# Optimization experiments

Measured on AMD Instinct MI355X. Metric: run time of the kernel, lower is better.

The kernel has to match this reference:

```python
import jax, jax.numpy as jnp
import numpy as np

N_SIN = 3  # fcn_n_sin (static)


def setup_inputs() -> dict:
    key = jax.random.key(0)
    ks = jax.random.split(key, 5)
    B, I, O, H = 256, 128, 128, 32
    F = 1 + 2 * N_SIN
    return {
        "x": jax.random.normal(ks[0], (B, I), dtype=jnp.float32),
        "W1": jax.random.normal(ks[1], (I, O, H, F), dtype=jnp.float32) * 0.3,
        "W2": jax.random.normal(ks[2], (I, O, 1, H), dtype=jnp.float32) * 0.3,
        "B1": jax.random.normal(ks[3], (I, O, H), dtype=jnp.float32) * 0.1,
        "B2": jax.random.normal(ks[4], (I, O, 1), dtype=jnp.float32) * 0.1,
    }


def reference(x, W1, W2, B1, B2):
    # x: [B, I]; per-(i,o) edge MLP on a scalar input, summed over i.
    omega = (2.0 ** jnp.arange(N_SIN)).astype(x.dtype)          # [S]
    ox = x[..., None] * omega                                    # [B, I, S]
    feat = jnp.concatenate([x[..., None], jnp.sin(ox), jnp.cos(ox)], axis=-1)  # [B, I, 1+2S]
    # First linear: per-edge [F -> H]
    h = jnp.einsum('bif,iohf->bioh', feat, W1) + B1              # [B, I, O, H]
    h = jax.nn.silu(h)
    # Second linear: per-edge [H -> 1], then sum over input dims i
    out = jnp.einsum('bioh,ioh->bio', h, W2[:, :, 0, :]) + B2[:, :, 0]  # [B, I, O]
    return out.sum(axis=1)                                       # [B, O]
```

## Files before the change

kernel.cpp:

```cpp
#include <hip/hip_runtime.h>
#include <hip/hip_bf16.h>

#define B_DIM 256
#define I_DIM 128
#define O_DIM 128
#define H_DIM 32
#define F_DIM 7
#define ICHUNK 8
#define NCHUNK (I_DIM / ICHUNK)

typedef __attribute__((ext_vector_type(8))) short short8;
typedef __attribute__((ext_vector_type(4))) float float4v;

__device__ inline short bf16s(float v) {
    union { __hip_bfloat16 h; short s; } u;
    u.h = __float2bfloat16(v);
    return u.s;
}

template <bool USE_WS>
__global__ __launch_bounds__(256, 2)
void fcnkan_mfma(const float* __restrict__ x,
                 const float* __restrict__ W1,
                 const float* __restrict__ W2,
                 const float* __restrict__ B1,
                 const float* __restrict__ B2,
                 float* __restrict__ ws,
                 float* __restrict__ out) {
    __shared__ __align__(16) short feat_s[ICHUNK * B_DIM * 8];
    __shared__ __align__(16) short w1_s[ICHUNK * H_DIM * 8];
    __shared__ float b1_s[ICHUNK * H_DIM];
    __shared__ float w2_s[ICHUNK * H_DIM];

    const int tid  = threadIdx.x;
    const int o    = blockIdx.x;
    const int ic0  = blockIdx.y * ICHUNK;
    const int w    = tid >> 6;
    const int lane = tid & 63;
    const int m    = lane & 15;
    const int q    = lane >> 4;

    const short8 zero8 = {};

    {
        const float4* xp = reinterpret_cast<const float4*>(x + (size_t)tid * I_DIM + ic0);
        float4 x0 = xp[0], x1 = xp[1];
        float xr[8] = {x0.x, x0.y, x0.z, x0.w, x1.x, x1.y, x1.z, x1.w};
        #pragma unroll
        for (int il = 0; il < ICHUNK; ++il) {
            float xv = xr[il];
            float s1 = __sinf(xv), c1 = __cosf(xv);
            float s2 = 2.f * s1 * c1, c2 = 1.f - 2.f * s1 * s1;
            float s4 = 2.f * s2 * c2, c4 = 1.f - 2.f * s2 * s2;
            short8 a;
            a[0] = bf16s(xv); a[1] = bf16s(s1); a[2] = bf16s(s2); a[3] = bf16s(s4);
            a[4] = bf16s(c1); a[5] = bf16s(c2); a[6] = bf16s(c4); a[7] = 0;
            *reinterpret_cast<short8*>(feat_s + (il * B_DIM + tid) * 8) = a;
        }
    }
    {
        int il = tid >> 5, h = tid & 31;
        size_t iobase = (size_t)(ic0 + il) * O_DIM + o;
        const float* wr = W1 + iobase * (H_DIM * F_DIM) + h * F_DIM;
        short8 bfr;
        #pragma unroll
        for (int f = 0; f < F_DIM; ++f) bfr[f] = bf16s(wr[f]);
        bfr[7] = 0;
        *reinterpret_cast<short8*>(w1_s + tid * 8) = bfr;
        b1_s[tid] = B1[iobase * H_DIM + h];
        w2_s[tid] = W2[iobase * H_DIM + h];
    }
    __syncthreads();

    float acc[16];
    #pragma unroll
    for (int r = 0; r < 16; ++r) acc[r] = 0.f;

    #pragma unroll 1
    for (int il = 0; il < ICHUNK; ++il) {
        const short8* fS = reinterpret_cast<const short8*>(feat_s) + il * B_DIM;
        const short8* wS = reinterpret_cast<const short8*>(w1_s) + il * H_DIM;

        short8 afrag[4];
        #pragma unroll
        for (int t = 0; t < 4; ++t)
            afrag[t] = fS[w * 64 + t * 16 + m];

        short8 bfrag[2];
        float  b1v[2], w2v[2];
        #pragma unroll
        for (int nt = 0; nt < 2; ++nt) {
            int h = nt * 16 + m;
            short8 b = wS[h];
            bfrag[nt] = (q == 0) ? b : zero8;
            b1v[nt] = b1_s[il * H_DIM + h];
            w2v[nt] = w2_s[il * H_DIM + h];
        }

        #pragma unroll
        for (int nt = 0; nt < 2; ++nt) {
            float4v c0 = {b1v[nt], b1v[nt], b1v[nt], b1v[nt]};
            #pragma unroll
            for (int t = 0; t < 4; ++t) {
                float4v z = __builtin_amdgcn_mfma_f32_16x16x32_bf16(
                    afrag[t], bfrag[nt], c0, 0, 0, 0);
                #pragma unroll
                for (int r = 0; r < 4; ++r) {
                    float zz = z[r];
                    float sg = __builtin_amdgcn_rcpf(1.f + __expf(-zz));
                    acc[t * 4 + r] = fmaf(zz * sg, w2v[nt], acc[t * 4 + r]);
                }
            }
        }
    }

    #pragma unroll
    for (int r = 0; r < 16; ++r) {
        float v = acc[r];
        v += __shfl_xor(v, 1, 64);
        v += __shfl_xor(v, 2, 64);
        v += __shfl_xor(v, 4, 64);
        v += __shfl_xor(v, 8, 64);
        acc[r] = v;
    }

    float b2c = 0.f;
    for (int il = 0; il < ICHUNK; ++il) b2c += B2[(size_t)(ic0 + il) * O_DIM + o];

    if (m == 0) {
        if (USE_WS) {
            float* wsp = ws + ((size_t)blockIdx.y * O_DIM + o) * B_DIM;
            #pragma unroll
            for (int t = 0; t < 4; ++t)
                #pragma unroll
                for (int r = 0; r < 4; ++r)
                    wsp[w * 64 + t * 16 + q * 4 + r] = acc[t * 4 + r] + b2c;
        } else {
            #pragma unroll
            for (int t = 0; t < 4; ++t)
                #pragma unroll
                for (int r = 0; r < 4; ++r) {
                    int b = w * 64 + t * 16 + q * 4 + r;
                    atomicAdd(&out[(size_t)b * O_DIM + o], acc[t * 4 + r] + b2c);
                }
        }
    }
}

__global__ __launch_bounds__(256)
void reduce_kernel(const float* __restrict__ ws, float* __restrict__ out) {
    const int o = blockIdx.x;
    const int b = threadIdx.x;
    float s = 0.f;
    #pragma unroll
    for (int c = 0; c < NCHUNK; ++c)
        s += ws[((size_t)c * O_DIM + o) * B_DIM + b];
    out[(size_t)b * O_DIM + o] = s;
}

extern "C" void kernel_launch(void* const* d_in, const int* in_sizes, int n_in,
                              void* d_out, int out_size, void* d_ws, size_t ws_size,
                              hipStream_t stream) {
    const float* x  = (const float*)d_in[0];
    const float* W1 = (const float*)d_in[1];
    const float* W2 = (const float*)d_in[2];
    const float* B1 = (const float*)d_in[3];
    const float* B2 = (const float*)d_in[4];
    float* out = (float*)d_out;
    float* ws  = (float*)d_ws;

    const size_t ws_need = (size_t)NCHUNK * O_DIM * B_DIM * sizeof(float);
    dim3 grid(O_DIM, NCHUNK);
    if (ws_size >= ws_need) {
        fcnkan_mfma<true><<<grid, 256, 0, stream>>>(x, W1, W2, B1, B2, ws, out);
        reduce_kernel<<<O_DIM, B_DIM, 0, stream>>>(ws, out);
    } else {
        hipMemsetAsync(out, 0, (size_t)out_size * sizeof(float), stream);
        fcnkan_mfma<false><<<grid, 256, 0, stream>>>(x, W1, W2, B1, B2, ws, out);
    }
}
```

Baseline: 107.1 us.

## Precompute features in a separate kernel and fold exp scaling into weights

Moves the sin/cos feature computation out of each of the 2048 main blocks into a one-time feature kernel that writes bf16 features to workspace, so the main kernel reads them from global memory instead of recomputing them. With the large feature LDS buffer gone, occupancy is raised to 6 blocks per SM. The -log2e factor is folded into W1/B1 and -ln2 into W2, so SiLU uses a raw exp2 with no extra multiply. This adds a kernel launch and global feature reads, and slightly changes rounding because the scaled weights are quantised to bf16.

```diff
diff --git a/kernel.cpp b/kernel.cpp
--- a/kernel.cpp
+++ b/kernel.cpp
@@ -8,6 +8,8 @@
 #define F_DIM 7
 #define ICHUNK 8
 #define NCHUNK (I_DIM / ICHUNK)
+#define NLOG2E -1.4426950408889634f
+#define NLN2   -0.6931471805599453f
 
 typedef __attribute__((ext_vector_type(8))) short short8;
 typedef __attribute__((ext_vector_type(4))) float float4v;
@@ -18,16 +20,39 @@
     return u.s;
 }
 
-template <bool USE_WS>
-__global__ __launch_bounds__(256, 2)
-void fcnkan_mfma(const float* __restrict__ x,
-                 const float* __restrict__ W1,
-                 const float* __restrict__ W2,
-                 const float* __restrict__ B1,
-                 const float* __restrict__ B2,
-                 float* __restrict__ ws,
-                 float* __restrict__ out) {
-    __shared__ __align__(16) short feat_s[ICHUNK * B_DIM * 8];
+__device__ inline float exp2_fast(float u) {
+#if __has_builtin(__builtin_amdgcn_exp2f)
+    return __builtin_amdgcn_exp2f(u);
+#else
+    return exp2f(u);
+#endif
+}
+
+__device__ inline short8 feat_pack(float xv) {
+    float s1 = __sinf(xv), c1 = __cosf(xv);
+    float s2 = 2.f * s1 * c1, c2 = 1.f - 2.f * s1 * s1;
+    float s4 = 2.f * s2 * c2, c4 = 1.f - 2.f * s2 * s2;
+    short8 a;
+    a[0] = bf16s(xv); a[1] = bf16s(s1); a[2] = bf16s(s2); a[3] = bf16s(s4);
+    a[4] = bf16s(c1); a[5] = bf16s(c2); a[6] = bf16s(c4); a[7] = 0;
+    return a;
+}
+
+__global__ __launch_bounds__(256)
+void feat_kernel(const float* __restrict__ x, short* __restrict__ feat_g) {
+    const int i = blockIdx.x;
+    const int b = threadIdx.x;
+    float xv = x[(size_t)b * I_DIM + i];
+    *reinterpret_cast<short8*>(feat_g + ((size_t)i * B_DIM + b) * 8) = feat_pack(xv);
+}
+
+__global__ __launch_bounds__(256, 6)
+void fcnkan_ws(const short* __restrict__ feat_g,
+               const float* __restrict__ W1,
+               const float* __restrict__ W2,
+               const float* __restrict__ B1,
+               const float* __restrict__ B2,
+               float* __restrict__ ws) {
     __shared__ __align__(16) short w1_s[ICHUNK * H_DIM * 8];
     __shared__ float b1_s[ICHUNK * H_DIM];
     __shared__ float w2_s[ICHUNK * H_DIM];
@@ -43,20 +68,126 @@
     const short8 zero8 = {};
 
     {
+        int il = tid >> 5, h = tid & 31;
+        size_t iobase = (size_t)(ic0 + il) * O_DIM + o;
+        const float* wr = W1 + iobase * (H_DIM * F_DIM) + h * F_DIM;
+        short8 bfr;
+        #pragma unroll
+        for (int f = 0; f < F_DIM; ++f) bfr[f] = bf16s(wr[f] * NLOG2E);
+        bfr[7] = 0;
+        *reinterpret_cast<short8*>(w1_s + tid * 8) = bfr;
+        b1_s[tid] = B1[iobase * H_DIM + h] * NLOG2E;
+        w2_s[tid] = W2[iobase * H_DIM + h] * NLN2;
+    }
+    __syncthreads();
+
+    float acc[16];
+    #pragma unroll
+    for (int r = 0; r < 16; ++r) acc[r] = 0.f;
+
+    #pragma unroll 1
+    for (int il = 0; il < ICHUNK; ++il) {
+        const short8* fG = reinterpret_cast<const short8*>(feat_g)
+                           + (size_t)(ic0 + il) * B_DIM;
+        const short8* wS = reinterpret_cast<const short8*>(w1_s) + il * H_DIM;
+
+        short8 afrag[4];
+        #pragma unroll
+        for (int t = 0; t < 4; ++t)
+            afrag[t] = fG[w * 64 + t * 16 + m];
+
+        short8 bfrag[2];
+        float  b1v[2], w2v[2];
+        #pragma unroll
+        for (int nt = 0; nt < 2; ++nt) {
+            int h = nt * 16 + m;
+            short8 b = wS[h];
+            bfrag[nt] = (q == 0) ? b : zero8;
+            b1v[nt] = b1_s[il * H_DIM + h];
+            w2v[nt] = w2_s[il * H_DIM + h];
+        }
+
+        #pragma unroll
+        for (int nt = 0; nt < 2; ++nt) {
+            float4v c0 = {b1v[nt], b1v[nt], b1v[nt], b1v[nt]};
+            #pragma unroll
+            for (int t = 0; t < 4; ++t) {
+                float4v z = __builtin_amdgcn_mfma_f32_16x16x32_bf16(
+                    afrag[t], bfrag[nt], c0, 0, 0, 0);
+                #pragma unroll
+                for (int r = 0; r < 4; ++r) {
+                    float u = z[r];
+                    float e = exp2_fast(u);
+                    float sg = __builtin_amdgcn_rcpf(1.f + e);
+                    acc[t * 4 + r] = fmaf(u * sg, w2v[nt], acc[t * 4 + r]);
+                }
+            }
+        }
+    }
+
+    #pragma unroll
+    for (int r = 0; r < 16; ++r) {
+        float v = acc[r];
+        v += __shfl_xor(v, 1, 64);
+        v += __shfl_xor(v, 2, 64);
+        v += __shfl_xor(v, 4, 64);
+        v += __shfl_xor(v, 8, 64);
+        acc[r] = v;
+    }
+
+    float b2c = 0.f;
+    for (int il = 0; il < ICHUNK; ++il) b2c += B2[(size_t)(ic0 + il) * O_DIM + o];
+
+    if (m == 0) {
+        float* wsp = ws + ((size_t)blockIdx.y * O_DIM + o) * B_DIM;
+        #pragma unroll
+        for (int t = 0; t < 4; ++t)
+            #pragma unroll
+            for (int r = 0; r < 4; ++r)
+                wsp[w * 64 + t * 16 + q * 4 + r] = acc[t * 4 + r] + b2c;
+    }
+}
+
+__global__ __launch_bounds__(256)
+void reduce_kernel(const float* __restrict__ ws, float* __restrict__ out) {
+    const int o = blockIdx.x;
+    const int b = threadIdx.x;
+    float s = 0.f;
+    #pragma unroll
+    for (int c = 0; c < NCHUNK; ++c)
+        s += ws[((size_t)c * O_DIM + o) * B_DIM + b];
+    out[(size_t)b * O_DIM + o] = s;
+}
+
+__global__ __launch_bounds__(256, 2)
+void fcnkan_atomic(const float* __restrict__ x,
+                   const float* __restrict__ W1,
+                   const float* __restrict__ W2,
+                   const float* __restrict__ B1,
+                   const float* __restrict__ B2,
+                   float* __restrict__ out) {
+    __shared__ __align__(16) short feat_s[ICHUNK * B_DIM * 8];
+    __shared__ __align__(16) short w1_s[ICHUNK * H_DIM * 8];
+    __shared__ float b1_s[ICHUNK * H_DIM];
+    __shared__ float w2_s[ICHUNK * H_DIM];
+
+    const int tid  = threadIdx.x;
+    const int o    = blockIdx.x;
+    const int ic0  = blockIdx.y * ICHUNK;
+    const int w    = tid >> 6;
+    const int lane = tid & 63;
+    const int m    = lane & 15;
+    const int q    = lane >> 4;
+
+    const short8 zero8 = {};
+
+    {
         const float4* xp = reinterpret_cast<const float4*>(x + (size_t)tid * I_DIM + ic0);
         float4 x0 = xp[0], x1 = xp[1];
         float xr[8] = {x0.x, x0.y, x0.z, x0.w, x1.x, x1.y, x1.z, x1.w};
         #pragma unroll
-        for (int il = 0; il < ICHUNK; ++il) {
-            float xv = xr[il];
-            float s1 = __sinf(xv), c1 = __cosf(xv);
-            float s2 = 2.f * s1 * c1, c2 = 1.f - 2.f * s1 * s1;
-            float s4 = 2.f * s2 * c2, c4 = 1.f - 2.f * s2 * s2;
-            short8 a;
-            a[0] = bf16s(xv); a[1] = bf16s(s1); a[2] = bf16s(s2); a[3] = bf16s(s4);
-            a[4] = bf16s(c1); a[5] = bf16s(c2); a[6] = bf16s(c4); a[7] = 0;
-            *reinterpret_cast<short8*>(feat_s + (il * B_DIM + tid) * 8) = a;
-        }
+        for (int il = 0; il < ICHUNK; ++il)
+            *reinterpret_cast<short8*>(feat_s + (il * B_DIM + tid) * 8) = feat_pack(xr[il]);
     }
     {
         int il = tid >> 5, h = tid & 31;
@@ -128,34 +259,14 @@
     for (int il = 0; il < ICHUNK; ++il) b2c += B2[(size_t)(ic0 + il) * O_DIM + o];
 
     if (m == 0) {
-        if (USE_WS) {
-            float* wsp = ws + ((size_t)blockIdx.y * O_DIM + o) * B_DIM;
-            #pragma unroll
-            for (int t = 0; t < 4; ++t)
-                #pragma unroll
-                for (int r = 0; r < 4; ++r)
-                    wsp[w * 64 + t * 16 + q * 4 + r] = acc[t * 4 + r] + b2c;
-        } else {
-            #pragma unroll
-            for (int t = 0; t < 4; ++t)
-                #pragma unroll
-                for (int r = 0; r < 4; ++r) {
-                    int b = w * 64 + t * 16 + q * 4 + r;
-                    atomicAdd(&out[(size_t)b * O_DIM + o], acc[t * 4 + r] + b2c);
-                }
-        }
-    }
-}
-
-__global__ __launch_bounds__(256)
-void reduce_kernel(const float* __restrict__ ws, float* __restrict__ out) {
-    const int o = blockIdx.x;
-    const int b = threadIdx.x;
-    float s = 0.f;
-    #pragma unroll
-    for (int c = 0; c < NCHUNK; ++c)
-        s += ws[((size_t)c * O_DIM + o) * B_DIM + b];
-    out[(size_t)b * O_DIM + o] = s;
+        #pragma unroll
+        for (int t = 0; t < 4; ++t)
+            #pragma unroll
+            for (int r = 0; r < 4; ++r) {
+                int b = w * 64 + t * 16 + q * 4 + r;
+                atomicAdd(&out[(size_t)b * O_DIM + o], acc[t * 4 + r] + b2c);
+            }
+    }
 }
 
 extern "C" void kernel_launch(void* const* d_in, const int* in_sizes, int n_in,
@@ -169,13 +280,18 @@
     float* out = (float*)d_out;
     float* ws  = (float*)d_ws;
 
-    const size_t ws_need = (size_t)NCHUNK * O_DIM * B_DIM * sizeof(float);
+    const size_t part_bytes = (size_t)NCHUNK * O_DIM * B_DIM * sizeof(float);
+    const size_t feat_bytes = (size_t)I_DIM * B_DIM * 8 * sizeof(short);
+    const size_t ws_need = part_bytes + feat_bytes;
+
     dim3 grid(O_DIM, NCHUNK);
     if (ws_size >= ws_need) {
-        fcnkan_mfma<true><<<grid, 256, 0, stream>>>(x, W1, W2, B1, B2, ws, out);
+        short* feat_g = (short*)((char*)d_ws + part_bytes);
+        feat_kernel<<<I_DIM, B_DIM, 0, stream>>>(x, feat_g);
+        fcnkan_ws<<<grid, 256, 0, stream>>>(feat_g, W1, W2, B1, B2, ws);
         reduce_kernel<<<O_DIM, B_DIM, 0, stream>>>(ws, out);
     } else {
         hipMemsetAsync(out, 0, (size_t)out_size * sizeof(float), stream);
-        fcnkan_mfma<false><<<grid, 256, 0, stream>>>(x, W1, W2, B1, B2, ws, out);
-    }
-}
+        fcnkan_atomic<<<grid, 256, 0, stream>>>(x, W1, W2, B1, B2, out);
+    }
+}
```

After: 105.7 us. About the same (-1.3%).
